# Kernel optimization log

Hardware: AMD Instinct MI355X
Metric: run time of the kernel (lower is better)

## Reference

```python
import jax, jax.numpy as jnp
import numpy as np

PAD = 0

def setup_inputs() -> dict:
    key = jax.random.key(0)
    k1, k2, k3, k4 = jax.random.split(key, 4)
    B, S, F, V, H, D = 64, 256, 4, 50257, 768, 512
    words = jax.random.randint(k1, (B, S, F), 0, V, dtype=jnp.int64)  # pad_index=0 occurs rarely at random
    E = jax.random.normal(k2, (V, H), dtype=jnp.float32) * 0.02      # stand-in for transformer last_hidden_state producer
    W = jax.random.normal(k3, (H, D), dtype=jnp.float32) * 0.02      # FFN projection weight
    b = jax.random.normal(k4, (D,), dtype=jnp.float32) * 0.02
    return {"words": words, "E": E, "W": W, "b": b}

def reference(words, E, W, b):
    # words: [B, S, F] subword ids; mask out pad subwords
    mask = (words != PAD)                                  # [B,S,F] bool
    sub = E[words] * mask[..., None].astype(E.dtype)       # [B,S,F,H], pads zeroed
    cnt = mask.sum(-1).astype(E.dtype)                     # [B,S] subwords per word
    # segment-mean over the fix_len axis; fully-padded words -> 0 (matches pad_sequence(..., 0))
    word_emb = sub.sum(-2) / jnp.maximum(cnt, 1.0)[..., None]   # [B,S,H]
    word_emb = jnp.where((cnt > 0)[..., None], word_emb, 0.0)
    return word_emb @ W + b                                # [B,S,D]
```

## Files before the change

kernel.cpp:

```cpp
#include <hip/hip_runtime.h>
#include <hip/hip_bf16.h>

#define M_TOT 16384
#define K_TOT 768
#define N_TOT 512
#define BM 32
#define NT 12
#define NSLOT 96

typedef __attribute__((ext_vector_type(8))) __bf16 bf16x8;
typedef __attribute__((ext_vector_type(4))) float f32x4;

static __device__ __forceinline__ ushort f2bf(float x) {
  union { float f; unsigned int u; } v; v.f = x;
  unsigned int r = v.u + 0x7fffu + ((v.u >> 16) & 1u);
  return (ushort)(r >> 16);
}
static __device__ __forceinline__ unsigned pack2(float lo, float hi) {
  return (unsigned)f2bf(lo) | ((unsigned)f2bf(hi) << 16);
}

__global__ __launch_bounds__(256) void wt_kernel(const float* __restrict__ W,
                                                 ushort* __restrict__ Wt) {
  __shared__ float tile[64][65];
  const int t  = threadIdx.x;
  const int k0 = blockIdx.x * 64;
  const int n0 = blockIdx.y * 64;
#pragma unroll
  for (int i = 0; i < 4; ++i) {
    const int idx = t + i * 256;
    const int r = idx >> 4;
    const int c = (idx & 15) * 4;
    const float4 v =
        *reinterpret_cast<const float4*>(W + (size_t)(k0 + r) * N_TOT + n0 + c);
    tile[r][c + 0] = v.x; tile[r][c + 1] = v.y;
    tile[r][c + 2] = v.z; tile[r][c + 3] = v.w;
  }
  __syncthreads();
#pragma unroll
  for (int i = 0; i < 4; ++i) {
    const int idx = t + i * 256;
    const int rn = idx >> 4;
    const int ck = (idx & 15) * 4;
    ushort4 o;
    o.x = f2bf(tile[ck + 0][rn]);
    o.y = f2bf(tile[ck + 1][rn]);
    o.z = f2bf(tile[ck + 2][rn]);
    o.w = f2bf(tile[ck + 3][rn]);
    const int kg    = k0 + ck;
    const int chunk = kg >> 3;
    const int e0    = kg & 7;
    *reinterpret_cast<ushort4*>(
        &Wt[((size_t)chunk * N_TOT + n0 + rn) * 8 + e0]) = o;
  }
}

__global__ __launch_bounds__(256, 2) void fused_kernel(
    const int* __restrict__ words, const float* __restrict__ E,
    const ushort* __restrict__ Wt, const float* __restrict__ bias,
    float* __restrict__ out) {
  __shared__ ushort A_l[BM * NSLOT * 8];
  __shared__ int   eoff_l[BM][4];
  __shared__ float msk_l[BM][4];
  __shared__ float scl_l[BM];

  const int t    = threadIdx.x;
  const int lane = t & 63;
  const int w    = t >> 6;
  const int bm   = blockIdx.x;

  if (t < BM) {
    const int4 w4 =
        *reinterpret_cast<const int4*>(words + (size_t)(bm * BM + t) * 4);
    const int ids[4] = {w4.x, w4.y, w4.z, w4.w};
    float cnt = 0.f;
#pragma unroll
    for (int f = 0; f < 4; ++f) {
      eoff_l[t][f] = ids[f] * K_TOT;
      const float m = (ids[f] != 0) ? 1.f : 0.f;
      msk_l[t][f] = m;
      cnt += m;
    }
    scl_l[t] = (cnt > 0.f) ? (1.f / cnt) : 0.f;
  }
  __syncthreads();

  const int sr = t >> 3;
  const int ss = t & 7;
  const int sw = ss ^ (sr & 7);
  const float4* pf[4];
#pragma unroll
  for (int f = 0; f < 4; ++f)
    pf[f] = reinterpret_cast<const float4*>(E + eoff_l[sr][f] + ss * 8);
  const float m0 = msk_l[sr][0], m1 = msk_l[sr][1];
  const float m2 = msk_l[sr][2], m3 = msk_l[sr][3];
  const float scl = scl_l[sr];

#define A_LOAD(va, kt)                                                       \
  do {                                                                       \
    _Pragma("unroll") for (int f = 0; f < 4; ++f) {                          \
      va[2 * f + 0] = pf[f][(kt) * 16 + 0];                                  \
      va[2 * f + 1] = pf[f][(kt) * 16 + 1];                                  \
    }                                                                        \
  } while (0)

#define A_MATH(va, kt)                                                       \
  do {                                                                       \
    float s[8];                                                              \
    _Pragma("unroll") for (int j = 0; j < 4; ++j) {                          \
      s[j] = (va[0][j] * m0 + va[2][j] * m1 + va[4][j] * m2 + va[6][j] * m3) \
             * scl;                                                          \
      s[4 + j] =                                                             \
          (va[1][j] * m0 + va[3][j] * m1 + va[5][j] * m2 + va[7][j] * m3) *  \
          scl;                                                               \
    }                                                                        \
    uint4 o;                                                                 \
    o.x = pack2(s[0], s[1]); o.y = pack2(s[2], s[3]);                        \
    o.z = pack2(s[4], s[5]); o.w = pack2(s[6], s[7]);                        \
    *reinterpret_cast<uint4*>(&A_l[((sr) * NSLOT + (kt) * 8 + sw) * 8]) = o; \
  } while (0)

  {
    float4 vaA[8], vaB[8];
    A_LOAD(vaA, 0);
    A_LOAD(vaB, 1);
#pragma unroll
    for (int kt = 0; kt < NT; kt += 2) {
      A_MATH(vaA, kt);
      if (kt + 2 < NT) A_LOAD(vaA, kt + 2);
      A_MATH(vaB, kt + 1);
      if (kt + 3 < NT) A_LOAD(vaB, kt + 3);
    }
  }
#undef A_LOAD
#undef A_MATH
  __syncthreads();

  f32x4 acc[2][8];
#pragma unroll
  for (int m = 0; m < 2; ++m)
#pragma unroll
    for (int n = 0; n < 8; ++n) acc[m][n] = (f32x4){0.f, 0.f, 0.f, 0.f};

  const int colBase = w * 128 + (lane & 15);
  const int rsel    = lane & 15;
  const int ksel    = lane >> 4;

#pragma unroll 2
  for (int kt = 0; kt < NT; ++kt) {
#pragma unroll
    for (int kk = 0; kk < 2; ++kk) {
      const int ks = kk * 4 + ksel;
      bf16x8 af[2], bfr[8];
#pragma unroll
      for (int m = 0; m < 2; ++m) {
        const int row = m * 16 + rsel;
        af[m] = *reinterpret_cast<const bf16x8*>(
            &A_l[(row * NSLOT + kt * 8 + (ks ^ (row & 7))) * 8]);
      }
#pragma unroll
      for (int n = 0; n < 8; ++n) {
        bfr[n] = *reinterpret_cast<const bf16x8*>(
            &Wt[((size_t)(kt * 8 + ks) * N_TOT + colBase + n * 16) * 8]);
      }
#pragma unroll
      for (int m = 0; m < 2; ++m)
#pragma unroll
        for (int n = 0; n < 8; ++n)
          acc[m][n] = __builtin_amdgcn_mfma_f32_16x16x32_bf16(
              af[m], bfr[n], acc[m][n], 0, 0, 0);
    }
  }

  const int row0 = bm * BM + (ksel << 2);
#pragma unroll
  for (int n = 0; n < 8; ++n) {
    const float bv = bias[colBase + n * 16];
#pragma unroll
    for (int m = 0; m < 2; ++m) {
#pragma unroll
      for (int j = 0; j < 4; ++j) {
        __builtin_nontemporal_store(
            acc[m][n][j] + bv,
            &out[(size_t)(row0 + m * 16 + j) * N_TOT + colBase + n * 16]);
      }
    }
  }
}

extern "C" void kernel_launch(void* const* d_in, const int* in_sizes, int n_in,
                              void* d_out, int out_size, void* d_ws,
                              size_t ws_size, hipStream_t stream) {
  const int*   words = (const int*)d_in[0];
  const float* E     = (const float*)d_in[1];
  const float* W     = (const float*)d_in[2];
  const float* b     = (const float*)d_in[3];
  float* out = (float*)d_out;

  ushort* Wtws = (ushort*)d_ws;

  hipLaunchKernelGGL(wt_kernel, dim3(K_TOT / 64, N_TOT / 64), dim3(256), 0,
                     stream, W, Wtws);
  hipLaunchKernelGGL(fused_kernel, dim3(M_TOT / BM), dim3(256), 0, stream,
                     words, E, Wtws, b, out);
}
```

Baseline: 54.46 us.

## Pipeline gather of second row tile behind MFMA compute of first in 512-thread blocks

Each block now handles 64 rows as two 32-row sub-tiles using 512 threads (8 waves, 64 columns each). The embedding gather and averaging for the second sub-tile is interleaved with the MFMA loop over the first sub-tile, writing into a second LDS buffer. The intent is to hide the random-access gather latency behind matrix compute instead of serialising the two phases. In exchange, each wave loads Wt fragments twice as often per output column, and the grid shrinks to 256 blocks at one block per CU, which risks low occupancy and idle CUs.

```diff
diff --git a/kernel.cpp b/kernel.cpp
--- a/kernel.cpp
+++ b/kernel.cpp
@@ -4,7 +4,6 @@
 #define M_TOT 16384
 #define K_TOT 768
 #define N_TOT 512
-#define BM 32
 #define NT 12
 #define NSLOT 96
 
@@ -55,23 +54,24 @@
   }
 }
 
-__global__ __launch_bounds__(256, 2) void fused_kernel(
+__global__ __launch_bounds__(512, 1) void fused_kernel(
     const int* __restrict__ words, const float* __restrict__ E,
     const ushort* __restrict__ Wt, const float* __restrict__ bias,
     float* __restrict__ out) {
-  __shared__ ushort A_l[BM * NSLOT * 8];
-  __shared__ int   eoff_l[BM][4];
-  __shared__ float msk_l[BM][4];
-  __shared__ float scl_l[BM];
+  __shared__ ushort A0[32 * NSLOT * 8];
+  __shared__ ushort A1[32 * NSLOT * 8];
+  __shared__ int   eoff_l[64][4];
+  __shared__ float msk_l[64][4];
+  __shared__ float scl_l[64];
 
   const int t    = threadIdx.x;
   const int lane = t & 63;
   const int w    = t >> 6;
   const int bm   = blockIdx.x;
 
-  if (t < BM) {
+  if (t < 64) {
     const int4 w4 =
-        *reinterpret_cast<const int4*>(words + (size_t)(bm * BM + t) * 4);
+        *reinterpret_cast<const int4*>(words + (size_t)(bm * 64 + t) * 4);
     const int ids[4] = {w4.x, w4.y, w4.z, w4.w};
     float cnt = 0.f;
 #pragma unroll
@@ -85,107 +85,147 @@
   }
   __syncthreads();
 
-  const int sr = t >> 3;
-  const int ss = t & 7;
-  const int sw = ss ^ (sr & 7);
-  const float4* pf[4];
-#pragma unroll
-  for (int f = 0; f < 4; ++f)
-    pf[f] = reinterpret_cast<const float4*>(E + eoff_l[sr][f] + ss * 8);
-  const float m0 = msk_l[sr][0], m1 = msk_l[sr][1];
-  const float m2 = msk_l[sr][2], m3 = msk_l[sr][3];
-  const float scl = scl_l[sr];
-
-#define A_LOAD(va, kt)                                                       \
-  do {                                                                       \
+  const int sr  = t >> 4;
+  const int seg = t & 7;
+  const int ktb = (t >> 3) & 1;
+  const int sw  = seg ^ (sr & 7);
+
+  const float4* pf[2][4];
+#pragma unroll
+  for (int f = 0; f < 4; ++f) {
+    pf[0][f] = reinterpret_cast<const float4*>(E + eoff_l[sr][f] + seg * 8);
+    pf[1][f] =
+        reinterpret_cast<const float4*>(E + eoff_l[32 + sr][f] + seg * 8);
+  }
+  const float mk[2][4] = {
+      {msk_l[sr][0], msk_l[sr][1], msk_l[sr][2], msk_l[sr][3]},
+      {msk_l[32 + sr][0], msk_l[32 + sr][1], msk_l[32 + sr][2],
+       msk_l[32 + sr][3]}};
+  const float sc[2] = {scl_l[sr], scl_l[32 + sr]};
+
+  float4 vgA[8], vgB[8];
+
+#define G_LOAD(vg, S, g)                                                     \
+  do {                                                                       \
+    const int kt_ = 2 * (g) + ktb;                                           \
     _Pragma("unroll") for (int f = 0; f < 4; ++f) {                          \
-      va[2 * f + 0] = pf[f][(kt) * 16 + 0];                                  \
-      va[2 * f + 1] = pf[f][(kt) * 16 + 1];                                  \
-    }                                                                        \
-  } while (0)
-
-#define A_MATH(va, kt)                                                       \
-  do {                                                                       \
+      vg[2 * f + 0] = pf[S][f][kt_ * 16 + 0];                                \
+      vg[2 * f + 1] = pf[S][f][kt_ * 16 + 1];                                \
+    }                                                                        \
+  } while (0)
+
+#define G_MATH(vg, dst, S, g)                                                \
+  do {                                                                       \
+    const int kt_ = 2 * (g) + ktb;                                           \
     float s[8];                                                              \
     _Pragma("unroll") for (int j = 0; j < 4; ++j) {                          \
-      s[j] = (va[0][j] * m0 + va[2][j] * m1 + va[4][j] * m2 + va[6][j] * m3) \
-             * scl;                                                          \
-      s[4 + j] =                                                             \
-          (va[1][j] * m0 + va[3][j] * m1 + va[5][j] * m2 + va[7][j] * m3) *  \
-          scl;                                                               \
+      s[j] = (vg[0][j] * mk[S][0] + vg[2][j] * mk[S][1] +                    \
+              vg[4][j] * mk[S][2] + vg[6][j] * mk[S][3]) * sc[S];            \
+      s[4 + j] = (vg[1][j] * mk[S][0] + vg[3][j] * mk[S][1] +                \
+                  vg[5][j] * mk[S][2] + vg[7][j] * mk[S][3]) * sc[S];        \
     }                                                                        \
     uint4 o;                                                                 \
     o.x = pack2(s[0], s[1]); o.y = pack2(s[2], s[3]);                        \
     o.z = pack2(s[4], s[5]); o.w = pack2(s[6], s[7]);                        \
-    *reinterpret_cast<uint4*>(&A_l[((sr) * NSLOT + (kt) * 8 + sw) * 8]) = o; \
-  } while (0)
-
-  {
-    float4 vaA[8], vaB[8];
-    A_LOAD(vaA, 0);
-    A_LOAD(vaB, 1);
-#pragma unroll
-    for (int kt = 0; kt < NT; kt += 2) {
-      A_MATH(vaA, kt);
-      if (kt + 2 < NT) A_LOAD(vaA, kt + 2);
-      A_MATH(vaB, kt + 1);
-      if (kt + 3 < NT) A_LOAD(vaB, kt + 3);
-    }
-  }
-#undef A_LOAD
-#undef A_MATH
-  __syncthreads();
-
-  f32x4 acc[2][8];
+    *reinterpret_cast<uint4*>(&(dst)[(sr * NSLOT + kt_ * 8 + sw) * 8]) = o;  \
+  } while (0)
+
+  const int rsel = lane & 15;
+  const int ksel = lane >> 4;
+  const int colBase = w * 64 + rsel;
+
+  f32x4 acc[2][4];
+
+#define COMPUTE(Asrc, kt)                                                    \
+  do {                                                                       \
+    _Pragma("unroll") for (int kk = 0; kk < 2; ++kk) {                       \
+      const int ks = kk * 4 + ksel;                                          \
+      bf16x8 af[2], bfr[4];                                                  \
+      _Pragma("unroll") for (int m = 0; m < 2; ++m) {                        \
+        const int r = m * 16 + rsel;                                         \
+        af[m] = *reinterpret_cast<const bf16x8*>(                            \
+            &(Asrc)[(r * NSLOT + (kt) * 8 + (ks ^ (r & 7))) * 8]);           \
+      }                                                                      \
+      _Pragma("unroll") for (int n = 0; n < 4; ++n)                          \
+        bfr[n] = *reinterpret_cast<const bf16x8*>(                           \
+            &Wt[((size_t)((kt) * 8 + ks) * N_TOT + colBase + n * 16) * 8]);  \
+      _Pragma("unroll") for (int m = 0; m < 2; ++m)                          \
+        _Pragma("unroll") for (int n = 0; n < 4; ++n)                        \
+          acc[m][n] = __builtin_amdgcn_mfma_f32_16x16x32_bf16(               \
+              af[m], bfr[n], acc[m][n], 0, 0, 0);                            \
+    }                                                                        \
+  } while (0)
+
+#define EPILOGUE(T)                                                          \
+  do {                                                                       \
+    const int row0 = bm * 64 + (T) * 32 + (ksel << 2);                       \
+    _Pragma("unroll") for (int n = 0; n < 4; ++n) {                          \
+      const float bv = bias[colBase + n * 16];                               \
+      _Pragma("unroll") for (int m = 0; m < 2; ++m) {                        \
+        _Pragma("unroll") for (int j = 0; j < 4; ++j) {                      \
+          __builtin_nontemporal_store(                                       \
+              acc[m][n][j] + bv,                                             \
+              &out[(size_t)(row0 + m * 16 + j) * N_TOT + colBase + n * 16]); \
+        }                                                                    \
+      }                                                                      \
+    }                                                                        \
+  } while (0)
+
+  G_LOAD(vgA, 0, 0);
+  G_LOAD(vgB, 0, 1);
+  G_MATH(vgA, A0, 0, 0);  G_LOAD(vgA, 0, 2);
+  G_MATH(vgB, A0, 0, 1);  G_LOAD(vgB, 0, 3);
+  G_MATH(vgA, A0, 0, 2);  G_LOAD(vgA, 0, 4);
+  G_MATH(vgB, A0, 0, 3);  G_LOAD(vgB, 0, 5);
+  G_MATH(vgA, A0, 0, 4);
+  G_MATH(vgB, A0, 0, 5);
+  __syncthreads();
+
 #pragma unroll
   for (int m = 0; m < 2; ++m)
 #pragma unroll
-    for (int n = 0; n < 8; ++n) acc[m][n] = (f32x4){0.f, 0.f, 0.f, 0.f};
-
-  const int colBase = w * 128 + (lane & 15);
-  const int rsel    = lane & 15;
-  const int ksel    = lane >> 4;
-
-#pragma unroll 2
-  for (int kt = 0; kt < NT; ++kt) {
-#pragma unroll
-    for (int kk = 0; kk < 2; ++kk) {
-      const int ks = kk * 4 + ksel;
-      bf16x8 af[2], bfr[8];
-#pragma unroll
-      for (int m = 0; m < 2; ++m) {
-        const int row = m * 16 + rsel;
-        af[m] = *reinterpret_cast<const bf16x8*>(
-            &A_l[(row * NSLOT + kt * 8 + (ks ^ (row & 7))) * 8]);
-      }
-#pragma unroll
-      for (int n = 0; n < 8; ++n) {
-        bfr[n] = *reinterpret_cast<const bf16x8*>(
-            &Wt[((size_t)(kt * 8 + ks) * N_TOT + colBase + n * 16) * 8]);
-      }
-#pragma unroll
-      for (int m = 0; m < 2; ++m)
-#pragma unroll
-        for (int n = 0; n < 8; ++n)
-          acc[m][n] = __builtin_amdgcn_mfma_f32_16x16x32_bf16(
-              af[m], bfr[n], acc[m][n], 0, 0, 0);
-    }
-  }
-
-  const int row0 = bm * BM + (ksel << 2);
-#pragma unroll
-  for (int n = 0; n < 8; ++n) {
-    const float bv = bias[colBase + n * 16];
-#pragma unroll
-    for (int m = 0; m < 2; ++m) {
-#pragma unroll
-      for (int j = 0; j < 4; ++j) {
-        __builtin_nontemporal_store(
-            acc[m][n][j] + bv,
-            &out[(size_t)(row0 + m * 16 + j) * N_TOT + colBase + n * 16]);
-      }
-    }
-  }
+    for (int n = 0; n < 4; ++n) acc[m][n] = (f32x4){0.f, 0.f, 0.f, 0.f};
+
+  G_LOAD(vgA, 1, 0);
+  COMPUTE(A0, 0);
+  COMPUTE(A0, 1);
+  G_LOAD(vgB, 1, 1);
+  COMPUTE(A0, 2);
+  G_MATH(vgA, A1, 1, 0);
+  COMPUTE(A0, 3);
+  G_LOAD(vgA, 1, 2);
+  COMPUTE(A0, 4);
+  G_MATH(vgB, A1, 1, 1);
+  COMPUTE(A0, 5);
+  G_LOAD(vgB, 1, 3);
+  COMPUTE(A0, 6);
+  G_MATH(vgA, A1, 1, 2);
+  COMPUTE(A0, 7);
+  G_LOAD(vgA, 1, 4);
+  COMPUTE(A0, 8);
+  G_MATH(vgB, A1, 1, 3);
+  COMPUTE(A0, 9);
+  G_LOAD(vgB, 1, 5);
+  COMPUTE(A0, 10);
+  G_MATH(vgA, A1, 1, 4);
+  COMPUTE(A0, 11);
+  G_MATH(vgB, A1, 1, 5);
+
+  EPILOGUE(0);
+  __syncthreads();
+
+#pragma unroll
+  for (int m = 0; m < 2; ++m)
+#pragma unroll
+    for (int n = 0; n < 4; ++n) acc[m][n] = (f32x4){0.f, 0.f, 0.f, 0.f};
+#pragma unroll
+  for (int kt = 0; kt < NT; ++kt) COMPUTE(A1, kt);
+  EPILOGUE(1);
+
+#undef G_LOAD
+#undef G_MATH
+#undef COMPUTE
+#undef EPILOGUE
 }
 
 extern "C" void kernel_launch(void* const* d_in, const int* in_sizes, int n_in,
@@ -201,6 +241,6 @@
 
   hipLaunchKernelGGL(wt_kernel, dim3(K_TOT / 64, N_TOT / 64), dim3(256), 0,
                      stream, W, Wtws);
-  hipLaunchKernelGGL(fused_kernel, dim3(M_TOT / BM), dim3(256), 0, stream,
+  hipLaunchKernelGGL(fused_kernel, dim3(M_TOT / 64), dim3(512), 0, stream,
                      words, E, Wtws, b, out);
 }
```

Result: no change. 54.21 us (-0.4%).

## Halve row tile to 16, remap gather threads, fully unroll MFMA loop with setprio

Applied to the files above, without the earlier changes.

Reduces the M tile from 32 to 16 rows, so the grid doubles to 1024 blocks and each wave keeps one A fragment and 8 accumulators. The gather stage is remapped so 16 threads cover each row, with six explicit software-pipelined groups. The MFMA K loop is fully unrolled and wrapped in s_setprio. The aim is more parallelism and better latency hiding on the gather-bound work. In exchange, each block now reuses every Wt fragment it loads for half as many rows, doubling Wt global traffic, and the launch-bounds occupancy hint is dropped.

```diff
diff --git a/kernel.cpp b/kernel.cpp
--- a/kernel.cpp
+++ b/kernel.cpp
@@ -4,7 +4,7 @@
 #define M_TOT 16384
 #define K_TOT 768
 #define N_TOT 512
-#define BM 32
+#define BM 16
 #define NT 12
 #define NSLOT 96
 
@@ -55,7 +55,7 @@
   }
 }
 
-__global__ __launch_bounds__(256, 2) void fused_kernel(
+__global__ __launch_bounds__(256) void fused_kernel(
     const int* __restrict__ words, const float* __restrict__ E,
     const ushort* __restrict__ Wt, const float* __restrict__ bias,
     float* __restrict__ out) {
@@ -85,90 +85,84 @@
   }
   __syncthreads();
 
-  const int sr = t >> 3;
-  const int ss = t & 7;
-  const int sw = ss ^ (sr & 7);
+  const int sr  = t >> 4;
+  const int c16 = t & 15;
   const float4* pf[4];
 #pragma unroll
   for (int f = 0; f < 4; ++f)
-    pf[f] = reinterpret_cast<const float4*>(E + eoff_l[sr][f] + ss * 8);
+    pf[f] = reinterpret_cast<const float4*>(E + eoff_l[sr][f]);
   const float m0 = msk_l[sr][0], m1 = msk_l[sr][1];
   const float m2 = msk_l[sr][2], m3 = msk_l[sr][3];
   const float scl = scl_l[sr];
 
-#define A_LOAD(va, kt)                                                       \
+  float4 vgA[8], vgB[8];
+
+#define G_LOAD(vg, g)                                                        \
   do {                                                                       \
+    const int s_ = c16 + 16 * (g);                                           \
     _Pragma("unroll") for (int f = 0; f < 4; ++f) {                          \
-      va[2 * f + 0] = pf[f][(kt) * 16 + 0];                                  \
-      va[2 * f + 1] = pf[f][(kt) * 16 + 1];                                  \
+      vg[2 * f + 0] = pf[f][s_ * 2 + 0];                                     \
+      vg[2 * f + 1] = pf[f][s_ * 2 + 1];                                     \
     }                                                                        \
   } while (0)
 
-#define A_MATH(va, kt)                                                       \
+#define G_MATH(vg, g)                                                        \
   do {                                                                       \
+    const int s_  = c16 + 16 * (g);                                          \
+    const int kt_ = s_ >> 3;                                                 \
+    const int sw_ = (s_ & 7) ^ (sr & 7);                                     \
     float s[8];                                                              \
     _Pragma("unroll") for (int j = 0; j < 4; ++j) {                          \
-      s[j] = (va[0][j] * m0 + va[2][j] * m1 + va[4][j] * m2 + va[6][j] * m3) \
+      s[j] = (vg[0][j] * m0 + vg[2][j] * m1 + vg[4][j] * m2 + vg[6][j] * m3) \
              * scl;                                                          \
       s[4 + j] =                                                             \
-          (va[1][j] * m0 + va[3][j] * m1 + va[5][j] * m2 + va[7][j] * m3) *  \
+          (vg[1][j] * m0 + vg[3][j] * m1 + vg[5][j] * m2 + vg[7][j] * m3) *  \
           scl;                                                               \
     }                                                                        \
     uint4 o;                                                                 \
     o.x = pack2(s[0], s[1]); o.y = pack2(s[2], s[3]);                        \
     o.z = pack2(s[4], s[5]); o.w = pack2(s[6], s[7]);                        \
-    *reinterpret_cast<uint4*>(&A_l[((sr) * NSLOT + (kt) * 8 + sw) * 8]) = o; \
+    *reinterpret_cast<uint4*>(                                               \
+        &A_l[(sr * NSLOT + kt_ * 8 + sw_) * 8]) = o;                         \
   } while (0)
 
-  {
-    float4 vaA[8], vaB[8];
-    A_LOAD(vaA, 0);
-    A_LOAD(vaB, 1);
-#pragma unroll
-    for (int kt = 0; kt < NT; kt += 2) {
-      A_MATH(vaA, kt);
-      if (kt + 2 < NT) A_LOAD(vaA, kt + 2);
-      A_MATH(vaB, kt + 1);
-      if (kt + 3 < NT) A_LOAD(vaB, kt + 3);
-    }
-  }
-#undef A_LOAD
-#undef A_MATH
+  G_LOAD(vgA, 0);  G_LOAD(vgB, 1);
+  G_MATH(vgA, 0);  G_LOAD(vgA, 2);
+  G_MATH(vgB, 1);  G_LOAD(vgB, 3);
+  G_MATH(vgA, 2);  G_LOAD(vgA, 4);
+  G_MATH(vgB, 3);  G_LOAD(vgB, 5);
+  G_MATH(vgA, 4);
+  G_MATH(vgB, 5);
+#undef G_LOAD
+#undef G_MATH
   __syncthreads();
 
-  f32x4 acc[2][8];
+  f32x4 acc[8];
 #pragma unroll
-  for (int m = 0; m < 2; ++m)
+  for (int n = 0; n < 8; ++n) acc[n] = (f32x4){0.f, 0.f, 0.f, 0.f};
+
+  const int rsel = lane & 15;
+  const int ksel = lane >> 4;
+  const int colBase = w * 128 + rsel;
+
 #pragma unroll
-    for (int n = 0; n < 8; ++n) acc[m][n] = (f32x4){0.f, 0.f, 0.f, 0.f};
-
-  const int colBase = w * 128 + (lane & 15);
-  const int rsel    = lane & 15;
-  const int ksel    = lane >> 4;
-
-#pragma unroll 2
   for (int kt = 0; kt < NT; ++kt) {
 #pragma unroll
     for (int kk = 0; kk < 2; ++kk) {
       const int ks = kk * 4 + ksel;
-      bf16x8 af[2], bfr[8];
+      const bf16x8 af = *reinterpret_cast<const bf16x8*>(
+          &A_l[(rsel * NSLOT + kt * 8 + (ks ^ (rsel & 7))) * 8]);
+      bf16x8 bfr[8];
 #pragma unroll
-      for (int m = 0; m < 2; ++m) {
-        const int row = m * 16 + rsel;
-        af[m] = *reinterpret_cast<const bf16x8*>(
-            &A_l[(row * NSLOT + kt * 8 + (ks ^ (row & 7))) * 8]);
-      }
-#pragma unroll
-      for (int n = 0; n < 8; ++n) {
+      for (int n = 0; n < 8; ++n)
         bfr[n] = *reinterpret_cast<const bf16x8*>(
             &Wt[((size_t)(kt * 8 + ks) * N_TOT + colBase + n * 16) * 8]);
-      }
+      __builtin_amdgcn_s_setprio(1);
 #pragma unroll
-      for (int m = 0; m < 2; ++m)
-#pragma unroll
-        for (int n = 0; n < 8; ++n)
-          acc[m][n] = __builtin_amdgcn_mfma_f32_16x16x32_bf16(
-              af[m], bfr[n], acc[m][n], 0, 0, 0);
+      for (int n = 0; n < 8; ++n)
+        acc[n] = __builtin_amdgcn_mfma_f32_16x16x32_bf16(af, bfr[n], acc[n],
+                                                         0, 0, 0);
+      __builtin_amdgcn_s_setprio(0);
     }
   }
 
@@ -177,13 +171,10 @@
   for (int n = 0; n < 8; ++n) {
     const float bv = bias[colBase + n * 16];
 #pragma unroll
-    for (int m = 0; m < 2; ++m) {
-#pragma unroll
-      for (int j = 0; j < 4; ++j) {
-        __builtin_nontemporal_store(
-            acc[m][n][j] + bv,
-            &out[(size_t)(row0 + m * 16 + j) * N_TOT + colBase + n * 16]);
-      }
+    for (int j = 0; j < 4; ++j) {
+      __builtin_nontemporal_store(
+          acc[n][j] + bv,
+          &out[(size_t)(row0 + j) * N_TOT + colBase + n * 16]);
     }
   }
 }
```

Measured after the change: 64.41 us. 1.18x slower.
